# Performance work log

Measured on AMD Instinct MI355X. Metric: run time of the kernel, lower is better.

The kernel has to match this reference:

```python
import jax, jax.numpy as jnp
import numpy as np

N = 2048   # query length
M = 2048   # key length
B = 2      # batch
D = 1024   # model dim (d_x_q = d_x_kv = d_out)
H = 16     # heads
DQK = D // H
DV = D // H
OFFSET = 0


def setup_inputs() -> dict:
    key = jax.random.key(0)
    k1, k2, k3, k4, k5, k6 = jax.random.split(key, 6)
    return {
        "x_q": jax.random.normal(k1, (N, B, D), dtype=jnp.float32),
        "x_kv": jax.random.normal(k2, (M, B, D), dtype=jnp.float32),
        "to_q": jax.random.normal(k3, (H, DQK, D), dtype=jnp.float32),
        "to_kv": jax.random.normal(k4, (H, DQK + DV, D), dtype=jnp.float32),
        "for_pos_enc": jax.random.normal(k5, (H, DQK, D), dtype=jnp.float32),
        "to_o": jax.random.normal(k6, (D, H, DV), dtype=jnp.float32),
    }


def _pos_enc(for_pos_enc, n, m, offset, d_x_kv):
    # relative distances i - j + offset, range [offset-(m-1), offset+(n-1)]
    dmin = offset - (m - 1)
    dmax = offset + (n - 1)
    r = jnp.arange(dmin, dmax + 1, dtype=jnp.float32)            # [R]
    inv_freq = 1.0 / (10000.0 ** (jnp.arange(0.0, d_x_kv, 2.0, dtype=jnp.float32) / d_x_kv))
    phases = r[:, None] * inv_freq[None, :]                       # [R, d/2]
    sincos = jnp.concatenate([jnp.sin(phases), jnp.cos(phases)], axis=-1)  # [R, d]
    table = jnp.einsum('hdb,rb->rhd', for_pos_enc, sincos)       # [R, H, DQK]
    dists = jnp.arange(n)[:, None] - jnp.arange(m)[None, :] + offset
    return table[dists - dmin]                                    # [n, m, H, DQK]


def reference(x_q, x_kv, to_q, to_kv, for_pos_enc, to_o):
    d_qk = to_q.shape[1]
    q = jnp.einsum('hdb,nzb->nzhd', to_q, x_q)     # [N,B,H,DQK]
    kv = jnp.einsum('hdb,mzb->mzhd', to_kv, x_kv)  # [M,B,H,DQK+DV]
    k = kv[..., :d_qk]
    v = kv[..., d_qk:]
    n, m = x_q.shape[0], x_kv.shape[0]

    pos_enc = _pos_enc(for_pos_enc, n, m, OFFSET, x_kv.shape[-1])

    content_logits = jnp.einsum('nzhd,mzhd->nmzh', q, k)          # [N,M,B,H]
    position_logits = jnp.einsum('nzhd,nmhd->nmzh', q, pos_enc)   # [N,M,B,H]
    logits = content_logits + position_logits

    # causal mask: True above diagonal shifted by 1+offset
    mask = jnp.triu(jnp.ones((n, m), dtype=bool), 1 + OFFSET)
    logits = jnp.where(mask[:, :, None, None], -jnp.inf, logits)

    weights = jax.nn.softmax(logits, axis=1)
    attn = jnp.einsum('nmzh,mzhd->nzhd', weights, v)              # [N,B,H,DV]
    out = jnp.einsum('dhb,nzhb->nzd', to_o, attn)                 # [N,B,D]
    return out
```

## Files before the change

kernel.cpp:

```cpp
#include <hip/hip_runtime.h>
#include <math.h>

#define NQ 2048
#define MKV 2048
#define BZ 2
#define DM 1024
#define NH 16
#define DH 64
#define RTAB 4095
#define R0TAB 1984
#define MTAB (RTAB - R0TAB)
#define LOG2E 1.44269504088896340736f

typedef __bf16 bf16x8 __attribute__((ext_vector_type(8)));
typedef float f32x4 __attribute__((ext_vector_type(4)));

__device__ inline unsigned short f2bf(float x) {
  __bf16 b = (__bf16)x;
  union { __bf16 b; unsigned short u; } v; v.b = b; return v.u;
}
__device__ inline float bf2f(unsigned short h) {
  union { unsigned u; float f; } v; v.u = ((unsigned)h) << 16; return v.f;
}
__device__ inline float fexp2(float x) { return __builtin_amdgcn_exp2f(x); }

template <int N>
__device__ inline float ror16(float x) {
  union { float f; int i; } a, r;
  a.f = x;
  r.i = __builtin_amdgcn_mov_dpp(a.i, 0x120 | N, 0xf, 0xf, true);
  return r.f;
}
__device__ inline float rowmax16(float x) {
  x = fmaxf(x, ror16<1>(x));
  x = fmaxf(x, ror16<2>(x));
  x = fmaxf(x, ror16<4>(x));
  x = fmaxf(x, ror16<8>(x));
  return x;
}
__device__ inline float rowsum16(float x) {
  x += ror16<1>(x);
  x += ror16<2>(x);
  x += ror16<4>(x);
  x += ror16<8>(x);
  return x;
}

#define SWZ(r, b) ((b) ^ (((r) & 7) << 4))
#define VSWZ(dv, m) \
  ((dv) * 128 + (((((m) >> 3) ^ ((dv) & 7) ^ (((dv) >> 3) & 7)) << 4)) + ((m) & 7) * 2)

__device__ inline void gload_lds16(const void* g, void* l) {
  __builtin_amdgcn_global_load_lds((const __attribute__((address_space(1))) void*)g,
                                   (__attribute__((address_space(3))) void*)l, 16, 0, 0);
}

__global__ __launch_bounds__(256) void prep_kernel(
    const float* __restrict__ i0, unsigned short* __restrict__ h0, unsigned short* __restrict__ l0, int n0,
    const float* __restrict__ i1, unsigned short* __restrict__ h1, unsigned short* __restrict__ l1, int n1,
    const float* __restrict__ i2, unsigned short* __restrict__ h2, unsigned short* __restrict__ l2, int n2,
    const float* __restrict__ i3, unsigned short* __restrict__ h3, unsigned short* __restrict__ l3, int n3,
    const float* __restrict__ i4, unsigned short* __restrict__ h4, unsigned short* __restrict__ l4, int n4_,
    const float* __restrict__ i5, unsigned short* __restrict__ h5, unsigned short* __restrict__ l5, int n5,
    unsigned short* __restrict__ schi, unsigned short* __restrict__ sclo) {
  if (blockIdx.y == 6) {
    for (int idx = blockIdx.x * 256 + threadIdx.x; idx < MTAB * DM; idx += gridDim.x * 256) {
      int r = idx / DM;
      int b = idx - r * DM;
      int i = (b < DM / 2) ? b : (b - DM / 2);
      double fr = exp((double)i * (-9.210340371976184 / 512.0));
      float rr = (float)(R0TAB + r - (MKV - 1));
      float ph = rr * (float)fr;
      float val = (b < DM / 2) ? sinf(ph) : cosf(ph);
      unsigned short hb = f2bf(val);
      schi[idx] = hb;
      sclo[idx] = f2bf(val - bf2f(hb));
    }
    return;
  }
  const float* in; unsigned short* hp; unsigned short* lp; int n4;
  switch (blockIdx.y) {
    case 0: in = i0; hp = h0; lp = l0; n4 = n0; break;
    case 1: in = i1; hp = h1; lp = l1; n4 = n1; break;
    case 2: in = i2; hp = h2; lp = l2; n4 = n2; break;
    case 3: in = i3; hp = h3; lp = l3; n4 = n3; break;
    case 4: in = i4; hp = h4; lp = l4; n4 = n4_; break;
    default: in = i5; hp = h5; lp = l5; n4 = n5; break;
  }
  for (int i = blockIdx.x * 256 + threadIdx.x; i < n4; i += gridDim.x * 256) {
    float4 v = ((const float4*)in)[i];
    float f[4] = {v.x, v.y, v.z, v.w};
    ushort4 hq, lq;
    unsigned short* hh = (unsigned short*)&hq;
    unsigned short* ll = (unsigned short*)&lq;
#pragma unroll
    for (int e = 0; e < 4; ++e) {
      unsigned short hb = f2bf(f[e]);
      hh[e] = hb;
      ll[e] = f2bf(f[e] - bf2f(hb));
    }
    ((ushort4*)hp)[i] = hq;
    ((ushort4*)lp)[i] = lq;
  }
}

template <int SPLIT_OUT, int KVSKIP>
__device__ __forceinline__ void gemm_body(
    const unsigned short* __restrict__ Ahi, const unsigned short* __restrict__ Alo,
    const unsigned short* __restrict__ Bhi, const unsigned short* __restrict__ Blo,
    float* __restrict__ Cf, unsigned short* __restrict__ Chi, unsigned short* __restrict__ Clo,
    int M, int N, int row0, int col0, char* lds, float cscale) {
  const int K = 1024;
  char* sAh = lds;
  char* sAl = lds + 16384;
  char* sBh = lds + 32768;
  char* sBl = lds + 49152;
  const int t = threadIdx.x;
  const int w = t >> 6;
  const int lane = t & 63;
  const int lo = lane & 15;
  const int hi = lane >> 4;
  const int wm = w >> 1, wn = w & 1;

  f32x4 acc[4][4];
#pragma unroll
  for (int a = 0; a < 4; ++a)
#pragma unroll
    for (int b = 0; b < 4; ++b) acc[a][b] = (f32x4){0.f, 0.f, 0.f, 0.f};

  for (int k0 = 0; k0 < K; k0 += 64) {
#pragma unroll
    for (int i = 0; i < 4; ++i) {
      int L = i * 4096 + t * 16;
      int r = L >> 7;
      int c16 = (L >> 4) & 7;
      int g16 = c16 ^ (r & 7);
      int ra = row0 + r;
      if (ra >= M) ra = M - 1;
      int rb = col0 + r;
      const char* gah = (const char*)(Ahi + (size_t)ra * K + k0) + g16 * 16;
      const char* gal = (const char*)(Alo + (size_t)ra * K + k0) + g16 * 16;
      const char* gbh = (const char*)(Bhi + (size_t)rb * K + k0) + g16 * 16;
      const char* gbl = (const char*)(Blo + (size_t)rb * K + k0) + g16 * 16;
      gload_lds16(gah, sAh + L);
      gload_lds16(gal, sAl + L);
      gload_lds16(gbh, sBh + L);
      gload_lds16(gbl, sBl + L);
    }
    __syncthreads();
#pragma unroll
    for (int ks = 0; ks < 2; ++ks) {
      bf16x8 ah[4], al[4], bh[4], bl[4];
#pragma unroll
      for (int f = 0; f < 4; ++f) {
        int rA = wm * 64 + 16 * f + lo;
        int offA = rA * 128 + (((4 * ks + hi) ^ (rA & 7)) << 4);
        ah[f] = *(const bf16x8*)(sAh + offA);
        al[f] = *(const bf16x8*)(sAl + offA);
        int rB = wn * 64 + 16 * f + lo;
        int offB = rB * 128 + (((4 * ks + hi) ^ (rB & 7)) << 4);
        bh[f] = *(const bf16x8*)(sBh + offB);
        bl[f] = *(const bf16x8*)(sBl + offB);
      }
#pragma unroll
      for (int fm = 0; fm < 4; ++fm)
#pragma unroll
        for (int fn = 0; fn < 4; ++fn) {
          acc[fm][fn] = __builtin_amdgcn_mfma_f32_16x16x32_bf16(ah[fm], bh[fn], acc[fm][fn], 0, 0, 0);
          acc[fm][fn] = __builtin_amdgcn_mfma_f32_16x16x32_bf16(ah[fm], bl[fn], acc[fm][fn], 0, 0, 0);
          acc[fm][fn] = __builtin_amdgcn_mfma_f32_16x16x32_bf16(al[fm], bh[fn], acc[fm][fn], 0, 0, 0);
        }
    }
    __syncthreads();
  }
#pragma unroll
  for (int fm = 0; fm < 4; ++fm)
#pragma unroll
    for (int qq = 0; qq < 4; ++qq) {
      int row = row0 + wm * 64 + 16 * fm + 4 * hi + qq;
      if (row < M) {
#pragma unroll
        for (int fn = 0; fn < 4; ++fn) {
          int col = col0 + wn * 64 + 16 * fn + lo;
          float v = acc[fm][fn][qq] * cscale;
          if (SPLIT_OUT) {
            unsigned short hb = f2bf(v);
            Chi[(size_t)row * N + col] = hb;
            if (!KVSKIP || wn == 0)
              Clo[(size_t)row * N + col] = f2bf(v - bf2f(hb));
          } else {
            Cf[(size_t)row * N + col] = v;
          }
        }
      }
    }
}

__global__ __launch_bounds__(256, 2) void gemm3_kernel(
    const unsigned short* __restrict__ xqh, const unsigned short* __restrict__ xql,
    const unsigned short* __restrict__ tqh, const unsigned short* __restrict__ tql,
    unsigned short* __restrict__ qh, unsigned short* __restrict__ ql,
    const unsigned short* __restrict__ xkh, const unsigned short* __restrict__ xkl,
    const unsigned short* __restrict__ tkh, const unsigned short* __restrict__ tkl,
    unsigned short* __restrict__ kvh, unsigned short* __restrict__ kvl,
    const unsigned short* __restrict__ sch, const unsigned short* __restrict__ scl,
    const unsigned short* __restrict__ fph, const unsigned short* __restrict__ fpl,
    unsigned short* __restrict__ tbh, unsigned short* __restrict__ tbl) {
  __shared__ char lds[65536];
  int bx = blockIdx.x;
  if (bx < 256) {
    int gx = bx & 7, gy = bx >> 3;
    gemm_body<1, 0>(xqh, xql, tqh, tql, nullptr, qh, ql, 4096, 1024, gy * 128, gx * 128, lds, LOG2E);
  } else if (bx < 768) {
    bx -= 256;
    int gx = bx & 15, gy = bx >> 4;
    gemm_body<1, 1>(xkh, xkl, tkh, tkl, nullptr, kvh, kvl, 4096, 2048, gy * 128, gx * 128, lds, 1.0f);
  } else {
    bx -= 768;
    int gx = bx & 7, gy = bx >> 3;
    gemm_body<1, 0>(sch, scl, fph, fpl, nullptr, tbh, tbl, MTAB, 1024, gy * 128, gx * 128, lds, 1.0f);
  }
}

__global__ __launch_bounds__(256, 2) void gemm_out_kernel(
    const unsigned short* __restrict__ A,
    const unsigned short* __restrict__ B,
    float* __restrict__ C) {
  __shared__ __align__(16) char sA[8192];
  __shared__ __align__(16) char sB[16384];
  const int t = threadIdx.x;
  const int w = t >> 6;
  const int lane = t & 63;
  const int lo = lane & 15;
  const int hi = lane >> 4;
  const int row0 = blockIdx.y * 64;
  const int col0 = blockIdx.x * 128;

  f32x4 acc[4][2];
#pragma unroll
  for (int a = 0; a < 4; ++a)
#pragma unroll
    for (int b = 0; b < 2; ++b) acc[a][b] = (f32x4){0.f, 0.f, 0.f, 0.f};

  for (int k0 = 0; k0 < 1024; k0 += 64) {
#pragma unroll
    for (int it = 0; it < 2; ++it) {
      int f = it * 256 + t;
      int r = f >> 3;
      int c = f & 7;
      int g16 = c ^ (r & 7);
      gload_lds16(A + (size_t)(row0 + r) * 1024 + k0 + g16 * 8, sA + f * 16);
    }
#pragma unroll
    for (int it = 0; it < 4; ++it) {
      int f = it * 256 + t;
      int r = f >> 3;
      int c = f & 7;
      int g16 = c ^ (r & 7);
      gload_lds16(B + (size_t)(col0 + r) * 1024 + k0 + g16 * 8, sB + f * 16);
    }
    __syncthreads();
#pragma unroll
    for (int ks = 0; ks < 2; ++ks) {
      bf16x8 af[4], bf_[2];
#pragma unroll
      for (int f = 0; f < 4; ++f) {
        int rA = 16 * f + lo;
        af[f] = *(const bf16x8*)(sA + rA * 128 + (((4 * ks + hi) ^ (rA & 7)) << 4));
      }
#pragma unroll
      for (int f = 0; f < 2; ++f) {
        int rB = 32 * w + 16 * f + lo;
        bf_[f] = *(const bf16x8*)(sB + rB * 128 + (((4 * ks + hi) ^ (rB & 7)) << 4));
      }
#pragma unroll
      for (int fm = 0; fm < 4; ++fm)
#pragma unroll
        for (int fn = 0; fn < 2; ++fn)
          acc[fm][fn] = __builtin_amdgcn_mfma_f32_16x16x32_bf16(af[fm], bf_[fn], acc[fm][fn], 0, 0, 0);
    }
    __syncthreads();
  }
#pragma unroll
  for (int fm = 0; fm < 4; ++fm)
#pragma unroll
    for (int qq = 0; qq < 4; ++qq) {
      int row = row0 + 16 * fm + 4 * hi + qq;
#pragma unroll
      for (int fn = 0; fn < 2; ++fn)
        C[(size_t)row * 1024 + col0 + 32 * w + 16 * fn + lo] = acc[fm][fn][qq];
    }
}

union U8 { uint4 q; unsigned short u[8]; };

__global__ __launch_bounds__(256, 2) void attn_kernel(
    const unsigned short* __restrict__ qhi, const unsigned short* __restrict__ qlo,
    const unsigned short* __restrict__ kvhi, const unsigned short* __restrict__ kvlo,
    const unsigned short* __restrict__ tabhi, const unsigned short* __restrict__ tablo,
    unsigned short* __restrict__ ohi) {
  __shared__ __align__(16) char sKhi[8192];
  __shared__ __align__(16) char sKlo[8192];
  __shared__ __align__(16) char sT[32768];
  __shared__ __align__(16) char sVT[8192];
  __shared__ __align__(16) char sP[8192];

  const int t = threadIdx.x;
  const int w = t >> 6;
  const int lane = t & 63;
  const int lo = lane & 15;
  const int hi = lane >> 4;

  for (int rep = 0; rep < 2; ++rep) {
    const int item = rep == 0 ? (1023 - (int)blockIdx.x) : (int)blockIdx.x;
    const int qb = item >> 5;
    const int z = (item >> 4) & 1;
    const int h = item & 15;
    const int n0 = qb * 64;

    bf16x8 qh[2], ql[2];
    {
      size_t qoff = (size_t)((n0 + 16 * w + lo) * BZ + z) * DM + h * DH;
#pragma unroll
      for (int ks = 0; ks < 2; ++ks) {
        qh[ks] = *(const bf16x8*)(qhi + qoff + 32 * ks + 8 * hi);
        ql[ks] = *(const bf16x8*)(qlo + qoff + 32 * ks + 8 * hi);
      }
    }

    f32x4 accO[4];
#pragma unroll
    for (int f = 0; f < 4; ++f) accO[f] = (f32x4){0.f, 0.f, 0.f, 0.f};
    float mi[4], li[4];
#pragma unroll
    for (int qq = 0; qq < 4; ++qq) { mi[qq] = -1e30f; li[qq] = 0.f; }

    uint4 pVh[2];
#pragma unroll
    for (int it = 0; it < 2; ++it) {
      int f = it * 256 + t;
      int j = f >> 3;
      int d8 = (f & 7) << 3;
      size_t gb = (size_t)((0 + j) * BZ + z) * (NH * 2 * DH) + h * (2 * DH);
      pVh[it] = *(const uint4*)(kvhi + gb + DH + d8);
    }

    for (int mt = 0; mt <= qb; ++mt) {
      const int m0 = mt * 64;
      const int Wb = n0 - m0 + R0TAB;
      __syncthreads();

#pragma unroll
      for (int it = 0; it < 2; ++it) {
        int f = it * 256 + t;
        int j = f >> 3;
        int c = f & 7;
        int gsw = (c ^ (j & 7)) << 3;
        size_t gb = (size_t)((m0 + j) * BZ + z) * (NH * 2 * DH) + h * (2 * DH);
        gload_lds16(kvhi + gb + gsw, sKhi + f * 16);
        gload_lds16(kvlo + gb + gsw, sKlo + f * 16);
      }
      if (mt == 0) {
#pragma unroll
        for (int it = 0; it < 4; ++it) {
          int f = it * 256 + t;
          int rr = f >> 3;
          int c = f & 7;
          int g = Wb + rr;
          int gc = g < RTAB ? g : (RTAB - 1);
          int slot = g & 127;
          int gsw = (c ^ (g & 7)) << 3;
          size_t gb = (size_t)gc * DM + h * DH;
          gload_lds16(tabhi + gb + gsw, sT + slot * 128 + c * 16);
          gload_lds16(tablo + gb + gsw, sT + 16384 + slot * 128 + c * 16);
        }
      } else {
#pragma unroll
        for (int it = 0; it < 2; ++it) {
          int f = it * 256 + t;
          int rr = f >> 3;
          int c = f & 7;
          int g = Wb + rr;
          int slot = g & 127;
          int gsw = (c ^ (g & 7)) << 3;
          size_t gb = (size_t)g * DM + h * DH;
          gload_lds16(tabhi + gb + gsw, sT + slot * 128 + c * 16);
          gload_lds16(tablo + gb + gsw, sT + 16384 + slot * 128 + c * 16);
        }
      }

#pragma unroll
      for (int it = 0; it < 2; ++it) {
        int f = it * 256 + t;
        int j = f >> 3;
        int d8 = (f & 7) << 3;
        U8 vh;
        vh.q = pVh[it];
#pragma unroll
        for (int e = 0; e < 8; ++e) {
          int dv = d8 + e;
          *(unsigned short*)(sVT + VSWZ(dv, j)) = vh.u[e];
        }
      }
      if (mt < qb) {
        const int m0n = (mt + 1) * 64;
#pragma unroll
        for (int it = 0; it < 2; ++it) {
          int f = it * 256 + t;
          int j = f >> 3;
          int d8 = (f & 7) << 3;
          size_t gb = (size_t)((m0n + j) * BZ + z) * (NH * 2 * DH) + h * (2 * DH);
          pVh[it] = *(const uint4*)(kvhi + gb + DH + d8);
        }
      }
      __syncthreads();

      f32x4 accS[4], accPL[5];
#pragma unroll
      for (int f = 0; f < 4; ++f) accS[f] = (f32x4){0.f, 0.f, 0.f, 0.f};
#pragma unroll
      for (int f = 0; f < 5; ++f) accPL[f] = (f32x4){0.f, 0.f, 0.f, 0.f};
#pragma unroll
      for (int ks = 0; ks < 2; ++ks) {
#pragma unroll
        for (int fm = 0; fm < 4; ++fm) {
          int rb = SWZ(lo, (16 * fm + lo) * 128 + (32 * ks + 8 * hi) * 2);
          bf16x8 kh = *(const bf16x8*)(sKhi + rb);
          bf16x8 kl = *(const bf16x8*)(sKlo + rb);
          accS[fm] = __builtin_amdgcn_mfma_f32_16x16x32_bf16(qh[ks], kh, accS[fm], 0, 0, 0);
          accS[fm] = __builtin_amdgcn_mfma_f32_16x16x32_bf16(qh[ks], kl, accS[fm], 0, 0, 0);
          accS[fm] = __builtin_amdgcn_mfma_f32_16x16x32_bf16(ql[ks], kh, accS[fm], 0, 0, 0);
        }
#pragma unroll
        for (int fr = 0; fr < 5; ++fr) {
          int g = Wb + 16 * (w + fr) + lo;
          int rb = (g & 127) * 128 + (((4 * ks + hi) ^ (g & 7)) << 4);
          bf16x8 th = *(const bf16x8*)(sT + rb);
          bf16x8 tl = *(const bf16x8*)(sT + 16384 + rb);
          accPL[fr] = __builtin_amdgcn_mfma_f32_16x16x32_bf16(qh[ks], th, accPL[fr], 0, 0, 0);
          accPL[fr] = __builtin_amdgcn_mfma_f32_16x16x32_bf16(qh[ks], tl, accPL[fr], 0, 0, 0);
          accPL[fr] = __builtin_amdgcn_mfma_f32_16x16x32_bf16(ql[ks], th, accPL[fr], 0, 0, 0);
        }
      }

#pragma unroll
      for (int fm = 0; fm < 4; ++fm)
#pragma unroll
        for (int qq = 0; qq < 4; ++qq) {
          int rn = 4 * hi + qq + 63 - 16 * fm - lo;
          float va = __shfl(accPL[3 - fm][qq], rn & 15, 16);
          float vb = __shfl(accPL[4 - fm][qq], rn & 15, 16);
          accS[fm][qq] += (rn >> 4) == (3 - fm) ? va : vb;
        }

      if (mt == qb) {
#pragma unroll
        for (int fm = 0; fm < 4; ++fm)
#pragma unroll
          for (int qq = 0; qq < 4; ++qq)
            if (16 * fm + lo > 16 * w + 4 * hi + qq) accS[fm][qq] = -1e30f;
      }

#pragma unroll
      for (int qq = 0; qq < 4; ++qq) {
        float pm = fmaxf(fmaxf(accS[0][qq], accS[1][qq]), fmaxf(accS[2][qq], accS[3][qq]));
        pm = rowmax16(pm);
        float mn = fmaxf(mi[qq], pm);
        float a = fexp2(mi[qq] - mn);
        mi[qq] = mn;
        float rs = 0.f;
#pragma unroll
        for (int fm = 0; fm < 4; ++fm) {
          float p = fexp2(accS[fm][qq] - mn);
          accS[fm][qq] = p;
          rs += p;
        }
        rs = rowsum16(rs);
        li[qq] = li[qq] * a + rs;
#pragma unroll
        for (int f = 0; f < 4; ++f) accO[f][qq] *= a;
      }

#pragma unroll
      for (int fm = 0; fm < 4; ++fm)
#pragma unroll
        for (int qq = 0; qq < 4; ++qq) {
          int row = 16 * w + 4 * hi + qq;
          *(unsigned short*)(sP + SWZ(4 * hi + qq, row * 128 + (16 * fm + lo) * 2)) =
              f2bf(accS[fm][qq]);
        }

#pragma unroll
      for (int ks = 0; ks < 2; ++ks) {
        int ab = SWZ(lo, (16 * w + lo) * 128 + (32 * ks + 8 * hi) * 2);
        bf16x8 pa = *(const bf16x8*)(sP + ab);
#pragma unroll
        for (int fv = 0; fv < 4; ++fv) {
          int dv = 16 * fv + lo;
          int vb = dv * 128 + ((((4 * ks + hi) ^ (dv & 7) ^ ((dv >> 3) & 7))) << 4);
          bf16x8 vv = *(const bf16x8*)(sVT + vb);
          accO[fv] = __builtin_amdgcn_mfma_f32_16x16x32_bf16(pa, vv, accO[fv], 0, 0, 0);
        }
      }
    }

#pragma unroll
    for (int qq = 0; qq < 4; ++qq) {
      float inv = 1.0f / li[qq];
      int n = n0 + 16 * w + 4 * hi + qq;
#pragma unroll
      for (int fv = 0; fv < 4; ++fv) {
        size_t idx = (size_t)(n * BZ + z) * DM + h * DH + 16 * fv + lo;
        ohi[idx] = f2bf(accO[fv][qq] * inv);
      }
    }
  }
}

extern "C" void kernel_launch(void* const* d_in, const int* in_sizes, int n_in,
                              void* d_out, int out_size, void* d_ws, size_t ws_size,
                              hipStream_t stream) {
  const float* x_q   = (const float*)d_in[0];
  const float* x_kv  = (const float*)d_in[1];
  const float* to_q  = (const float*)d_in[2];
  const float* to_kv = (const float*)d_in[3];
  const float* fpe   = (const float*)d_in[4];
  const float* to_o  = (const float*)d_in[5];
  float* out = (float*)d_out;

  char* W = (char*)d_ws;
  size_t o = 0;
  auto alloc = [&](size_t bytes) { char* p = W + o; o += (bytes + 255) & ~(size_t)255; return p; };
  typedef unsigned short us;
  us* q_hi  = (us*)alloc((size_t)4096 * 1024 * 2);
  us* q_lo  = (us*)alloc((size_t)4096 * 1024 * 2);
  us* kv_hi = (us*)alloc((size_t)4096 * 2048 * 2);
  us* kv_lo = (us*)alloc((size_t)4096 * 2048 * 2);
  us* tab_hi = (us*)alloc((size_t)RTAB * 1024 * 2);
  us* tab_lo = (us*)alloc((size_t)RTAB * 1024 * 2);
  us* xq_hi = (us*)alloc((size_t)4096 * 1024 * 2);
  us* xq_lo = (us*)alloc((size_t)4096 * 1024 * 2);
  us* xkv_hi = (us*)alloc((size_t)4096 * 1024 * 2);
  us* xkv_lo = (us*)alloc((size_t)4096 * 1024 * 2);
  us* tq_hi  = (us*)alloc((size_t)1024 * 1024 * 2);
  us* tq_lo  = (us*)alloc((size_t)1024 * 1024 * 2);
  us* tkv_hi = (us*)alloc((size_t)2048 * 1024 * 2);
  us* tkv_lo = (us*)alloc((size_t)2048 * 1024 * 2);
  us* to_hi  = (us*)alloc((size_t)1024 * 1024 * 2);
  us* to_lo  = (us*)alloc((size_t)1024 * 1024 * 2);
  us* fpe_hi = (us*)alloc((size_t)1024 * 1024 * 2);
  us* fpe_lo = (us*)alloc((size_t)1024 * 1024 * 2);
  us* sc_hi  = (us*)alloc((size_t)MTAB * 1024 * 2);
  us* sc_lo  = (us*)alloc((size_t)MTAB * 1024 * 2);

  prep_kernel<<<dim3(4096, 7), 256, 0, stream>>>(
      x_q,   xq_hi,  xq_lo,  4096 * 1024 / 4,
      x_kv,  xkv_hi, xkv_lo, 4096 * 1024 / 4,
      to_q,  tq_hi,  tq_lo,  1024 * 1024 / 4,
      to_kv, tkv_hi, tkv_lo, 2048 * 1024 / 4,
      to_o,  to_hi,  to_lo,  1024 * 1024 / 4,
      fpe,   fpe_hi, fpe_lo, 1024 * 1024 / 4,
      sc_hi, sc_lo);

  gemm3_kernel<<<dim3(904), 256, 0, stream>>>(
      xq_hi, xq_lo, tq_hi, tq_lo, q_hi, q_lo,
      xkv_hi, xkv_lo, tkv_hi, tkv_lo, kv_hi, kv_lo,
      sc_hi, sc_lo, fpe_hi, fpe_lo,
      tab_hi + (size_t)R0TAB * 1024, tab_lo + (size_t)R0TAB * 1024);

  us* at_hi = xkv_hi;
  attn_kernel<<<dim3(512), 256, 0, stream>>>(q_hi, q_lo, kv_hi, kv_lo,
                                             tab_hi, tab_lo, at_hi);
  gemm_out_kernel<<<dim3(8, 64), 256, 0, stream>>>(at_hi, to_hi, out);
}
```

Measured before the change: 234.0 us.

## Prefetch next positional table window into a 192-row LDS ring buffer

The positional-encoding table ring in LDS grows from 128 to 192 rows per hi/lo half. The first 128 rows are loaded once per work item before the loop. Each iteration then issues the next 64-row table load after the barrier, so it overlaps the current tile's MFMA work instead of being waited on at the loop-top barrier. This raises LDS use per block from 64KB to 80KB, which could limit the two-blocks-per-CU occupancy, and adds a multiply-based modulo-192 for slot indexing.

```diff
diff --git a/kernel.cpp b/kernel.cpp
--- a/kernel.cpp
+++ b/kernel.cpp
@@ -23,6 +23,11 @@
   union { unsigned u; float f; } v; v.u = ((unsigned)h) << 16; return v.f;
 }
 __device__ inline float fexp2(float x) { return __builtin_amdgcn_exp2f(x); }
+
+__device__ inline int slot192(int G) {
+  int q3 = ((G >> 6) * 43691) >> 17;
+  return G - 192 * q3;
+}
 
 template <int N>
 __device__ inline float ror16(float x) {
@@ -301,7 +306,7 @@
     unsigned short* __restrict__ ohi) {
   __shared__ __align__(16) char sKhi[8192];
   __shared__ __align__(16) char sKlo[8192];
-  __shared__ __align__(16) char sT[32768];
+  __shared__ __align__(16) char sT[49152];
   __shared__ __align__(16) char sVT[8192];
   __shared__ __align__(16) char sP[8192];
 
@@ -318,6 +323,25 @@
     const int h = item & 15;
     const int n0 = qb * 64;
 
+    __syncthreads();
+
+    {
+#pragma unroll
+      for (int it = 0; it < 4; ++it) {
+        int f = it * 256 + t;
+        int rr = f >> 3;
+        int c = f & 7;
+        int G = n0 + rr;
+        int grow = R0TAB + G;
+        if (grow > RTAB - 1) grow = RTAB - 1;
+        int slot = slot192(G);
+        int gsw = (c ^ (G & 7)) << 3;
+        size_t gb = (size_t)grow * DM + h * DH;
+        gload_lds16(tabhi + gb + gsw, sT + slot * 128 + c * 16);
+        gload_lds16(tablo + gb + gsw, sT + 24576 + slot * 128 + c * 16);
+      }
+    }
+
     bf16x8 qh[2], ql[2];
     {
       size_t qoff = (size_t)((n0 + 16 * w + lo) * BZ + z) * DM + h * DH;
@@ -347,7 +371,7 @@
 
     for (int mt = 0; mt <= qb; ++mt) {
       const int m0 = mt * 64;
-      const int Wb = n0 - m0 + R0TAB;
+      const int Wg = n0 - m0;
       __syncthreads();
 
 #pragma unroll
@@ -360,34 +384,6 @@
         gload_lds16(kvhi + gb + gsw, sKhi + f * 16);
         gload_lds16(kvlo + gb + gsw, sKlo + f * 16);
       }
-      if (mt == 0) {
-#pragma unroll
-        for (int it = 0; it < 4; ++it) {
-          int f = it * 256 + t;
-          int rr = f >> 3;
-          int c = f & 7;
-          int g = Wb + rr;
-          int gc = g < RTAB ? g : (RTAB - 1);
-          int slot = g & 127;
-          int gsw = (c ^ (g & 7)) << 3;
-          size_t gb = (size_t)gc * DM + h * DH;
-          gload_lds16(tabhi + gb + gsw, sT + slot * 128 + c * 16);
-          gload_lds16(tablo + gb + gsw, sT + 16384 + slot * 128 + c * 16);
-        }
-      } else {
-#pragma unroll
-        for (int it = 0; it < 2; ++it) {
-          int f = it * 256 + t;
-          int rr = f >> 3;
-          int c = f & 7;
-          int g = Wb + rr;
-          int slot = g & 127;
-          int gsw = (c ^ (g & 7)) << 3;
-          size_t gb = (size_t)g * DM + h * DH;
-          gload_lds16(tabhi + gb + gsw, sT + slot * 128 + c * 16);
-          gload_lds16(tablo + gb + gsw, sT + 16384 + slot * 128 + c * 16);
-        }
-      }
 
 #pragma unroll
       for (int it = 0; it < 2; ++it) {
@@ -414,6 +410,21 @@
         }
       }
       __syncthreads();
+
+      if (mt < qb) {
+#pragma unroll
+        for (int it = 0; it < 2; ++it) {
+          int f = it * 256 + t;
+          int rr = f >> 3;
+          int c = f & 7;
+          int Gn = Wg - 64 + rr;
+          int slot = slot192(Gn);
+          int gsw = (c ^ (Gn & 7)) << 3;
+          size_t gb = (size_t)(R0TAB + Gn) * DM + h * DH;
+          gload_lds16(tabhi + gb + gsw, sT + slot * 128 + c * 16);
+          gload_lds16(tablo + gb + gsw, sT + 24576 + slot * 128 + c * 16);
+        }
+      }
 
       f32x4 accS[4], accPL[5];
 #pragma unroll
@@ -433,10 +444,10 @@
         }
 #pragma unroll
         for (int fr = 0; fr < 5; ++fr) {
-          int g = Wb + 16 * (w + fr) + lo;
-          int rb = (g & 127) * 128 + (((4 * ks + hi) ^ (g & 7)) << 4);
+          int G = Wg + 16 * (w + fr) + lo;
+          int rb = slot192(G) * 128 + (((4 * ks + hi) ^ (G & 7)) << 4);
           bf16x8 th = *(const bf16x8*)(sT + rb);
-          bf16x8 tl = *(const bf16x8*)(sT + 16384 + rb);
+          bf16x8 tl = *(const bf16x8*)(sT + 24576 + rb);
           accPL[fr] = __builtin_amdgcn_mfma_f32_16x16x32_bf16(qh[ks], th, accPL[fr], 0, 0, 0);
           accPL[fr] = __builtin_amdgcn_mfma_f32_16x16x32_bf16(qh[ks], tl, accPL[fr], 0, 0, 0);
           accPL[fr] = __builtin_amdgcn_mfma_f32_16x16x32_bf16(ql[ks], th, accPL[fr], 0, 0, 0);
```

Result: no change. 238.3 us (+1.8%).
